# Optimization experiments

Measured on AMD Instinct MI355X. Metric: run time of the kernel, lower is better.

Reference implementation:

```python
import jax, jax.numpy as jnp
import numpy as np

N_NODES = 50000
N_EDGES = 800000
D = 128
N_LAYERS = 3
EPS = 1e-5  # torch LayerNorm default


def _gcn_conv(x, src, dst, dinv, W, b):
    # PyG GCNConv: h = x @ W; out[i] = sum_{(s->i)} dinv[s]*dinv[i]*h[s] + dinv[i]^2*h[i] + b
    h = x @ W
    norm = dinv[src] * dinv[dst]                      # [E]
    msgs = h[src] * norm[:, None]                     # [E, D] gather
    agg = jax.ops.segment_sum(msgs, dst, num_segments=N_NODES)  # scatter-add
    agg = agg + h * (dinv * dinv)[:, None]            # self-loop term
    return agg + b


def _layer_norm(x, gamma, beta):
    mu = jnp.mean(x, axis=-1, keepdims=True)
    var = jnp.mean(jnp.square(x - mu), axis=-1, keepdims=True)
    return (x - mu) * jax.lax.rsqrt(var + EPS) * gamma + beta


def setup_inputs() -> dict:
    key = jax.random.key(0)
    ks = jax.random.split(key, 4)
    x = jax.random.normal(ks[0], (N_NODES, D), dtype=jnp.float32)
    edge_index = jax.random.randint(ks[1], (2, N_EDGES), 0, N_NODES, dtype=jnp.int64)
    Ws = jax.random.normal(ks[2], (N_LAYERS, D, D), dtype=jnp.float32) * (1.0 / np.sqrt(D))
    bs = jnp.zeros((N_LAYERS, D), dtype=jnp.float32)
    gammas = jnp.ones((N_LAYERS, D), dtype=jnp.float32)
    betas = jnp.zeros((N_LAYERS, D), dtype=jnp.float32)
    return {"x": x, "edge_index": edge_index, "Ws": Ws, "bs": bs,
            "gammas": gammas, "betas": betas}


def reference(x, edge_index, Ws, bs, gammas, betas):
    src, dst = edge_index[0], edge_index[1]
    # GCN symmetric normalization with self-loops: deg[i] = in-degree(i) + 1
    deg = jnp.zeros((N_NODES,), dtype=x.dtype).at[dst].add(1.0) + 1.0
    dinv = jax.lax.rsqrt(deg)
    h = x
    for i in range(N_LAYERS):
        x_new = _gcn_conv(h, src, dst, dinv, Ws[i], bs[i])
        x_new = _layer_norm(x_new, gammas[i], betas[i])
        x_new = jax.nn.relu(x_new)  # dropout is identity in eval mode
        h = h + x_new if i > 0 else x_new
    return h
```

## Files before the change

### kernel.cpp

```cpp
#include <hip/hip_runtime.h>
#include <hip/hip_bf16.h>

#define NN 50000
#define NE 800000
#define DD 128
#define NB 196
#define CHSZ 6250
#define NSB 49
#define PH (64 * NB)
#define FS 2048
#define NSL 391
#define HHB (NSL * 8)
#define QB 3125
#define WB 192
#define LG 3125
#define LN_EPS 1e-5f

typedef __bf16 bf16x8 __attribute__((ext_vector_type(8)));
typedef float f32x4 __attribute__((ext_vector_type(4)));

__device__ inline ushort f2bf_bits(float f) {
    union { __hip_bfloat16 h; ushort u; } c;
    c.h = __float2bfloat16(f);
    return c.u;
}

__device__ inline void accum_q16(float* acc, uint4 v, float ww) {
    uint q0 = v.x, q1 = v.y, q2 = v.z, q3 = v.w;
    acc[0]  = fmaf(ww, (float)(char)(q0), acc[0]);
    acc[1]  = fmaf(ww, (float)(char)(q0 >> 8), acc[1]);
    acc[2]  = fmaf(ww, (float)(char)(q0 >> 16), acc[2]);
    acc[3]  = fmaf(ww, (float)(char)(q0 >> 24), acc[3]);
    acc[4]  = fmaf(ww, (float)(char)(q1), acc[4]);
    acc[5]  = fmaf(ww, (float)(char)(q1 >> 8), acc[5]);
    acc[6]  = fmaf(ww, (float)(char)(q1 >> 16), acc[6]);
    acc[7]  = fmaf(ww, (float)(char)(q1 >> 24), acc[7]);
    acc[8]  = fmaf(ww, (float)(char)(q2), acc[8]);
    acc[9]  = fmaf(ww, (float)(char)(q2 >> 8), acc[9]);
    acc[10] = fmaf(ww, (float)(char)(q2 >> 16), acc[10]);
    acc[11] = fmaf(ww, (float)(char)(q2 >> 24), acc[11]);
    acc[12] = fmaf(ww, (float)(char)(q3), acc[12]);
    acc[13] = fmaf(ww, (float)(char)(q3 >> 8), acc[13]);
    acc[14] = fmaf(ww, (float)(char)(q3 >> 16), acc[14]);
    acc[15] = fmaf(ww, (float)(char)(q3 >> 24), acc[15]);
}

__global__ void hist_cast_kernel(const int* __restrict__ dst, int* __restrict__ counts,
                                 int* __restrict__ rank, const float* __restrict__ x,
                                 uint2* __restrict__ qf0, float* __restrict__ sc0,
                                 const float* __restrict__ W, ushort* __restrict__ Wt) {
    int b = blockIdx.x;
    if (b < HHB) {
        int slice = b >> 3;
        int r = b & 7;
        int base = slice * FS;
#pragma unroll 2
        for (int i = threadIdx.x; i < FS; i += 256) {
            int e = base + i;
            if (e < NE) {
                int d = dst[e];
                if (d / CHSZ == r) rank[e] = atomicAdd(&counts[d], 1);
            }
        }
    } else if (b < HHB + QB) {
        int bb = b - HHB;
        int group = threadIdx.x >> 4, t = threadIdx.x & 15;
        int node = bb * 16 + group;
        const float4* xr = (const float4*)(x + (size_t)node * DD + t * 8);
        float4 v0 = xr[0], v1 = xr[1];
        float vals[8] = {v0.x, v0.y, v0.z, v0.w, v1.x, v1.y, v1.z, v1.w};
        float am = 0.f;
#pragma unroll
        for (int i = 0; i < 8; ++i) am = fmaxf(am, fabsf(vals[i]));
#pragma unroll
        for (int off = 1; off <= 8; off <<= 1) am = fmaxf(am, __shfl_xor(am, off, 64));
        float inv = 127.f / fmaxf(am, 1e-20f);
        uint lo = 0, hi = 0;
#pragma unroll
        for (int i = 0; i < 4; ++i) {
            int q = __float2int_rn(vals[i] * inv);
            lo |= ((uint)(q & 0xff)) << (8 * i);
        }
#pragma unroll
        for (int i = 0; i < 4; ++i) {
            int q = __float2int_rn(vals[4 + i] * inv);
            hi |= ((uint)(q & 0xff)) << (8 * i);
        }
        uint2 pk; pk.x = lo; pk.y = hi;
        qf0[node * 16 + t] = pk;
        if (t == 0) sc0[node] = am / 127.f;
    } else {
        int i = (b - HHB - QB) * 256 + threadIdx.x;
        int l = i >> 14, k = (i >> 7) & 127, n = i & 127;
        Wt[l * 16384 + n * 128 + k] = f2bf_bits(W[i]);
    }
}

__global__ __launch_bounds__(1024) void scan1024_blocks(int* __restrict__ data,
                                                        int* __restrict__ bsums) {
    __shared__ int ws[16];
    int gid = blockIdx.x * 1024 + threadIdx.x;
    int lane = threadIdx.x & 63, wid = threadIdx.x >> 6;
    int v = (gid < NN) ? data[gid] : 0;
    int x = v;
#pragma unroll
    for (int off = 1; off < 64; off <<= 1) {
        int t = __shfl_up(x, off, 64);
        if (lane >= off) x += t;
    }
    if (lane == 63) ws[wid] = x;
    __syncthreads();
    if (threadIdx.x == 0) {
        int run = 0;
        for (int i = 0; i < 16; ++i) { int t = ws[i]; ws[i] = run; run += t; }
        bsums[blockIdx.x] = run;
    }
    __syncthreads();
    if (gid < NN) data[gid] = x - v + ws[wid];
}

__global__ __launch_bounds__(1024) void scan_sums1024(int* __restrict__ bsums, int nb) {
    __shared__ int ws[16];
    int tid = threadIdx.x;
    int lane = tid & 63, wid = tid >> 6;
    int v = (tid < nb) ? bsums[tid] : 0;
    int x = v;
#pragma unroll
    for (int off = 1; off < 64; off <<= 1) {
        int t = __shfl_up(x, off, 64);
        if (lane >= off) x += t;
    }
    if (lane == 63) ws[wid] = x;
    __syncthreads();
    if (tid == 0) {
        int run = 0;
        for (int i = 0; i < 16; ++i) { int t = ws[i]; ws[i] = run; run += t; }
    }
    __syncthreads();
    if (tid < nb) bsums[tid] = x - v + ws[wid];
}

__global__ void finalize_kernel(const int* __restrict__ excl, const int* __restrict__ bsums,
                                int* __restrict__ row_ptr, float* __restrict__ dinv,
                                int* __restrict__ degarr, int* __restrict__ bh) {
    __shared__ int lh[64];
    if (threadIdx.x < 64) lh[threadIdx.x] = 0;
    __syncthreads();
    int d = blockIdx.x * 256 + threadIdx.x;
    if (d < NN) {
        int p0 = excl[d] + bsums[d >> 10];
        int nxt = (d == NN - 1) ? NE : excl[d + 1] + bsums[(d + 1) >> 10];
        int deg = nxt - p0;
        row_ptr[d] = p0;
        dinv[d] = rsqrtf((float)deg + 1.0f);
        degarr[d] = deg;
        atomicAdd(&lh[63 - min(deg, 63)], 1);
    }
    __syncthreads();
    if (threadIdx.x < 64) bh[threadIdx.x * NB + blockIdx.x] = lh[threadIdx.x];
    if (blockIdx.x == 0 && threadIdx.x == 0) row_ptr[NN] = NE;
}

__global__ __launch_bounds__(1024) void permscan_kernel(int* __restrict__ bh) {
    __shared__ int wsum[16];
    const int CH = 13;
    int tid = threadIdx.x;
    int base = tid * CH;
    int vals[CH];
    int s = 0;
#pragma unroll
    for (int i = 0; i < CH; ++i) {
        int idx = base + i;
        int v = (idx < PH) ? bh[idx] : 0;
        vals[i] = s;
        s += v;
    }
    int lane = tid & 63, wid = tid >> 6;
    int x = s;
#pragma unroll
    for (int off = 1; off < 64; off <<= 1) {
        int t = __shfl_up(x, off, 64);
        if (lane >= off) x += t;
    }
    if (lane == 63) wsum[wid] = x;
    __syncthreads();
    if (tid == 0) {
        int run = 0;
        for (int i = 0; i < 16; ++i) { int t = wsum[i]; wsum[i] = run; run += t; }
    }
    __syncthreads();
    int texcl = x - s + wsum[wid];
#pragma unroll
    for (int i = 0; i < CH; ++i) {
        int idx = base + i;
        if (idx < PH) bh[idx] = texcl + vals[i];
    }
}

__global__ void scatter_fill_kernel(const int* __restrict__ degarr, const int* __restrict__ bh,
                                    int* __restrict__ perm, const int* __restrict__ src,
                                    const int* __restrict__ dst, const int* __restrict__ excl,
                                    const int* __restrict__ bsums, const int* __restrict__ rank,
                                    const float* __restrict__ dinv, int2* __restrict__ edge2) {
    if (blockIdx.x < NB) {
        __shared__ int lh[64];
        __shared__ int lbase[64];
        if (threadIdx.x < 64) {
            lh[threadIdx.x] = 0;
            lbase[threadIdx.x] = bh[threadIdx.x * NB + blockIdx.x];
        }
        __syncthreads();
        int gid = blockIdx.x * 256 + threadIdx.x;
        if (gid < NN) {
            int b = 63 - min(degarr[gid], 63);
            int r = atomicAdd(&lh[b], 1);
            perm[lbase[b] + r] = gid;
        }
    } else {
        int bb = blockIdx.x - NB;
        if (bb == 0 && threadIdx.x < 8) {
            int2 z; z.x = 0; z.y = 0;
            edge2[NE + threadIdx.x] = z;
        }
        int slice = bb >> 3;
        int r = bb & 7;
        int base = slice * FS;
#pragma unroll 2
        for (int i = threadIdx.x; i < FS; i += 256) {
            int e = base + i;
            if (e < NE) {
                int d = dst[e];
                if (d / CHSZ == r) {
                    int s = src[e];
                    int pos = excl[d] + bsums[d >> 10] + rank[e];
                    int2 o;
                    o.x = s;
                    o.y = __float_as_int(dinv[s] * dinv[d]);
                    edge2[pos] = o;
                }
            }
        }
    }
}

template <bool RES, bool FINAL>
__global__ __launch_bounds__(128) void layer_kernel(
    const uint4* __restrict__ qin, const float* __restrict__ scin,
    const ushort* __restrict__ fin, const int* __restrict__ row_ptr,
    const int2* __restrict__ edge2, const int* __restrict__ perm,
    const float* __restrict__ dinv, const ushort* __restrict__ Wt,
    const float* __restrict__ bias, const float* __restrict__ gamma,
    const float* __restrict__ beta, ushort* __restrict__ fout, char* __restrict__ qfout,
    float* __restrict__ scout, float* __restrict__ out) {
    __shared__ uint4 sA[16 * 17];
    __shared__ int sNode[16];
    __shared__ float sLN1[2][16], sLN2[2][16];
    __shared__ float sMX[2][16];

    int tid = threadIdx.x;
    int wv = tid >> 6, lane = tid & 63;
    int grp = lane >> 3, ln = lane & 7;
    int arow = wv * 8 + grp;
    int slot = blockIdx.x * 16 + arow;
    int node = perm[slot];
    if (ln == 0) sNode[arow] = node;

    {
        int beg = row_ptr[node], deg = row_ptr[node + 1] - beg;
        int nbt = (deg + 7) >> 3;
        float acc[16] = {};

        uint4 qself = qin[node * 8 + ln];
        float wself = dinv[node];
        wself = wself * wself * scin[node];

        const int2* eb = edge2 + beg;
        int bsel = lane & 56;
        for (int b = 0; b < nbt; ++b) {
            int lim = deg - b * 8;
            int2 a = eb[b * 8 + ln];
            float wf = __int_as_float(a.y) * scin[a.x];
            int sj[8];
            float W8[8];
#pragma unroll
            for (int j = 0; j < 8; ++j) sj[j] = __shfl(a.x, bsel + j, 64);
#pragma unroll
            for (int j = 0; j < 8; ++j) W8[j] = __shfl(wf, bsel + j, 64);
            uint4 Q[8];
#pragma unroll
            for (int j = 0; j < 8; ++j) Q[j] = qin[sj[j] * 8 + ln];
#pragma unroll
            for (int j = 0; j < 8; ++j) accum_q16(acc, Q[j], (j < lim) ? W8[j] : 0.f);
        }
        accum_q16(acc, qself, wself);

        union { ushort us[16]; uint4 u[2]; } pk;
#pragma unroll
        for (int i = 0; i < 16; ++i) pk.us[i] = f2bf_bits(acc[i]);
        sA[arow * 17 + 2 * ln] = pk.u[0];
        sA[arow * 17 + 2 * ln + 1] = pk.u[1];
    }
    __syncthreads();

    int q4 = lane >> 4, m = lane & 15;
    f32x4 c0 = (f32x4){0.f, 0.f, 0.f, 0.f};
    f32x4 c1 = c0, c2 = c0, c3 = c0;
    int ncb = 64 * wv;
#pragma unroll
    for (int kk = 0; kk < 4; ++kk) {
        bf16x8 af = *(const bf16x8*)&sA[m * 17 + kk * 4 + q4];
        const ushort* wb = Wt + (size_t)(ncb + m) * DD + kk * 32 + q4 * 8;
        c0 = __builtin_amdgcn_mfma_f32_16x16x32_bf16(af, *(const bf16x8*)(wb), c0, 0, 0, 0);
        c1 = __builtin_amdgcn_mfma_f32_16x16x32_bf16(af, *(const bf16x8*)(wb + 16 * DD), c1, 0, 0, 0);
        c2 = __builtin_amdgcn_mfma_f32_16x16x32_bf16(af, *(const bf16x8*)(wb + 32 * DD), c2, 0, 0, 0);
        c3 = __builtin_amdgcn_mfma_f32_16x16x32_bf16(af, *(const bf16x8*)(wb + 48 * DD), c3, 0, 0, 0);
    }

    float bb0 = bias[ncb + m], bb1 = bias[ncb + 16 + m];
    float bb2 = bias[ncb + 32 + m], bb3 = bias[ncb + 48 + m];
    float s1[4], s2[4];
#pragma unroll
    for (int r = 0; r < 4; ++r) {
        float v0 = c0[r] + bb0, v1 = c1[r] + bb1, v2 = c2[r] + bb2, v3 = c3[r] + bb3;
        c0[r] = v0; c1[r] = v1; c2[r] = v2; c3[r] = v3;
        s1[r] = (v0 + v1) + (v2 + v3);
        s2[r] = (v0 * v0 + v1 * v1) + (v2 * v2 + v3 * v3);
    }
#pragma unroll
    for (int off = 1; off <= 8; off <<= 1) {
#pragma unroll
        for (int r = 0; r < 4; ++r) {
            s1[r] += __shfl_xor(s1[r], off, 64);
            s2[r] += __shfl_xor(s2[r], off, 64);
        }
    }
    if (m == 0) {
#pragma unroll
        for (int r = 0; r < 4; ++r) {
            sLN1[wv][q4 * 4 + r] = s1[r];
            sLN2[wv][q4 * 4 + r] = s2[r];
        }
    }
    __syncthreads();
    float ga0 = gamma[ncb + m], ga1 = gamma[ncb + 16 + m];
    float ga2 = gamma[ncb + 32 + m], ga3 = gamma[ncb + 48 + m];
    float be0 = beta[ncb + m], be1 = beta[ncb + 16 + m];
    float be2 = beta[ncb + 32 + m], be3 = beta[ncb + 48 + m];
    float o0v[4], o1v[4], o2v[4], o3v[4], rmax[4];
#pragma unroll
    for (int r = 0; r < 4; ++r) {
        int row = q4 * 4 + r;
        float S1 = sLN1[0][row] + sLN1[1][row];
        float S2 = sLN2[0][row] + sLN2[1][row];
        float mu = S1 * (1.f / 128.f);
        float var = S2 * (1.f / 128.f) - mu * mu;
        float rstd = rsqrtf(var + LN_EPS);
        int nd = sNode[row];
        size_t rb = (size_t)nd * DD;
        float o0 = fmaxf((c0[r] - mu) * rstd * ga0 + be0, 0.f);
        float o1 = fmaxf((c1[r] - mu) * rstd * ga1 + be1, 0.f);
        float o2 = fmaxf((c2[r] - mu) * rstd * ga2 + be2, 0.f);
        float o3 = fmaxf((c3[r] - mu) * rstd * ga3 + be3, 0.f);
        if (RES) {
            o0 += __uint_as_float(((uint)fin[rb + ncb + m]) << 16);
            o1 += __uint_as_float(((uint)fin[rb + ncb + 16 + m]) << 16);
            o2 += __uint_as_float(((uint)fin[rb + ncb + 32 + m]) << 16);
            o3 += __uint_as_float(((uint)fin[rb + ncb + 48 + m]) << 16);
        }
        if (FINAL) {
            out[rb + ncb + m] = o0;
            out[rb + ncb + 16 + m] = o1;
            out[rb + ncb + 32 + m] = o2;
            out[rb + ncb + 48 + m] = o3;
        } else {
            fout[rb + ncb + m] = f2bf_bits(o0);
            fout[rb + ncb + 16 + m] = f2bf_bits(o1);
            fout[rb + ncb + 32 + m] = f2bf_bits(o2);
            fout[rb + ncb + 48 + m] = f2bf_bits(o3);
            o0v[r] = o0; o1v[r] = o1; o2v[r] = o2; o3v[r] = o3;
            rmax[r] = fmaxf(fmaxf(o0, o1), fmaxf(o2, o3));
        }
    }
    if (!FINAL) {
#pragma unroll
        for (int off = 1; off <= 8; off <<= 1) {
#pragma unroll
            for (int r = 0; r < 4; ++r) rmax[r] = fmaxf(rmax[r], __shfl_xor(rmax[r], off, 64));
        }
        if (m == 0) {
#pragma unroll
            for (int r = 0; r < 4; ++r) sMX[wv][q4 * 4 + r] = rmax[r];
        }
        __syncthreads();
#pragma unroll
        for (int r = 0; r < 4; ++r) {
            int row = q4 * 4 + r;
            float M = fmaxf(sMX[0][row], sMX[1][row]);
            float inv = 127.f / fmaxf(M, 1e-20f);
            int nd = sNode[row];
            if (wv == 0 && m == 0) scout[nd] = M / 127.f;
            size_t rb = (size_t)nd * DD;
            int q0 = min(__float2int_rn(o0v[r] * inv), 127);
            int q1 = min(__float2int_rn(o1v[r] * inv), 127);
            int q2 = min(__float2int_rn(o2v[r] * inv), 127);
            int q3 = min(__float2int_rn(o3v[r] * inv), 127);
            qfout[rb + ncb + m] = (char)q0;
            qfout[rb + ncb + 16 + m] = (char)q1;
            qfout[rb + ncb + 32 + m] = (char)q2;
            qfout[rb + ncb + 48 + m] = (char)q3;
        }
    }
}


extern "C" void kernel_launch(void* const* d_in, const int* in_sizes, int n_in,
                              void* d_out, int out_size, void* d_ws, size_t ws_size,
                              hipStream_t stream) {
    const float* x = (const float*)d_in[0];
    const int* edge = (const int*)d_in[1];
    const float* Ws = (const float*)d_in[2];
    const float* bs = (const float*)d_in[3];
    const float* gs = (const float*)d_in[4];
    const float* bes = (const float*)d_in[5];
    float* out = (float*)d_out;
    const int* src = edge;
    const int* dst = edge + NE;

    char* p = (char*)d_ws;
    int* counts = (int*)p;      p += (size_t)NN * 4;
    int* bsums = (int*)p;       p += 1024 * 4;
    int* row_ptr = (int*)p;     p += (size_t)(NN + 4) * 4;
    int* rank = (int*)p;        p += (size_t)NE * 4;
    float* dinv = (float*)p;    p += (size_t)NN * 4;
    int* degarr = (int*)p;      p += (size_t)NN * 4;
    int* bh = (int*)p;          p += (size_t)PH * 4;
    int* perm = (int*)p;        p += (size_t)NN * 4;
    int2* edge2 = (int2*)p;     p += (size_t)(NE + 8) * 8;
    ushort* fb0 = (ushort*)p;   p += (size_t)NN * DD * 2;
    ushort* fb1 = (ushort*)p;   p += (size_t)NN * DD * 2;
    char* qf0 = (char*)p;       p += (size_t)NN * DD;
    char* qf1 = (char*)p;       p += (size_t)NN * DD;
    float* sc0 = (float*)p;     p += (size_t)NN * 4;
    float* sc1 = (float*)p;     p += (size_t)NN * 4;
    ushort* Wt = (ushort*)p;    p += (size_t)3 * DD * DD * 2;

    hipMemsetAsync(counts, 0, (size_t)NN * 4, stream);
    hist_cast_kernel<<<HHB + QB + WB, 256, 0, stream>>>(dst, counts, rank, x,
                                                        (uint2*)qf0, sc0, Ws, Wt);
    scan1024_blocks<<<NSB, 1024, 0, stream>>>(counts, bsums);
    scan_sums1024<<<1, 1024, 0, stream>>>(bsums, NSB);
    finalize_kernel<<<NB, 256, 0, stream>>>(counts, bsums, row_ptr, dinv, degarr, bh);
    permscan_kernel<<<1, 1024, 0, stream>>>(bh);
    scatter_fill_kernel<<<NB + NSL * 8, 256, 0, stream>>>(degarr, bh, perm, src, dst, counts,
                                                          bsums, rank, dinv, edge2);

    layer_kernel<false, false><<<LG, 128, 0, stream>>>(
        (const uint4*)qf0, sc0, fb0, row_ptr, edge2, perm, dinv, Wt, bs, gs, bes,
        fb1, qf1, sc1, out);
    layer_kernel<true, false><<<LG, 128, 0, stream>>>(
        (const uint4*)qf1, sc1, fb1, row_ptr, edge2, perm, dinv, Wt + 16384, bs + DD, gs + DD,
        bes + DD, fb0, qf0, sc0, out);
    layer_kernel<true, true><<<LG, 128, 0, stream>>>(
        (const uint4*)qf0, sc0, fb0, row_ptr, edge2, perm, dinv, Wt + 32768, bs + 2 * DD,
        gs + 2 * DD, bes + 2 * DD, fb1, qf1, sc1, out);
}
```

Measured before the change: 289.8 us.

## Switch int8 feature quantization from per-node to global per-tensor scale

Replaces the per-node int8 scale with a single per-tensor max-abs scale, computed by atomicMax reductions. The gather loop no longer loads a per-neighbor scale, and the scale is applied once to the accumulator before the bf16 conversion. Quantization now runs in separate quant kernels that read the bf16 features after each layer, which adds extra launches and an extra pass over memory. A global scale coarsens precision for rows with small magnitudes, so accuracy becomes a risk.

```diff
diff --git a/kernel.cpp b/kernel.cpp
--- a/kernel.cpp
+++ b/kernel.cpp
@@ -11,7 +11,7 @@
 #define FS 2048
 #define NSL 391
 #define HHB (NSL * 8)
-#define QB 3125
+#define AB 256
 #define WB 192
 #define LG 3125
 #define LN_EPS 1e-5f
@@ -47,8 +47,9 @@
 
 __global__ void hist_cast_kernel(const int* __restrict__ dst, int* __restrict__ counts,
                                  int* __restrict__ rank, const float* __restrict__ x,
-                                 uint2* __restrict__ qf0, float* __restrict__ sc0,
-                                 const float* __restrict__ W, ushort* __restrict__ Wt) {
+                                 int* __restrict__ amax0, const float* __restrict__ W,
+                                 ushort* __restrict__ Wt) {
+    __shared__ float sam[4];
     int b = blockIdx.x;
     if (b < HHB) {
         int slice = b >> 3;
@@ -62,38 +63,78 @@
                 if (d / CHSZ == r) rank[e] = atomicAdd(&counts[d], 1);
             }
         }
-    } else if (b < HHB + QB) {
+    } else if (b < HHB + AB) {
         int bb = b - HHB;
-        int group = threadIdx.x >> 4, t = threadIdx.x & 15;
-        int node = bb * 16 + group;
-        const float4* xr = (const float4*)(x + (size_t)node * DD + t * 8);
-        float4 v0 = xr[0], v1 = xr[1];
-        float vals[8] = {v0.x, v0.y, v0.z, v0.w, v1.x, v1.y, v1.z, v1.w};
+        const float4* xv = (const float4*)x;
         float am = 0.f;
-#pragma unroll
-        for (int i = 0; i < 8; ++i) am = fmaxf(am, fabsf(vals[i]));
-#pragma unroll
-        for (int off = 1; off <= 8; off <<= 1) am = fmaxf(am, __shfl_xor(am, off, 64));
-        float inv = 127.f / fmaxf(am, 1e-20f);
-        uint lo = 0, hi = 0;
-#pragma unroll
-        for (int i = 0; i < 4; ++i) {
-            int q = __float2int_rn(vals[i] * inv);
-            lo |= ((uint)(q & 0xff)) << (8 * i);
-        }
-#pragma unroll
-        for (int i = 0; i < 4; ++i) {
-            int q = __float2int_rn(vals[4 + i] * inv);
-            hi |= ((uint)(q & 0xff)) << (8 * i);
-        }
-        uint2 pk; pk.x = lo; pk.y = hi;
-        qf0[node * 16 + t] = pk;
-        if (t == 0) sc0[node] = am / 127.f;
+        for (int i = bb * 256 + threadIdx.x; i < NN * DD / 4; i += AB * 256) {
+            float4 v = xv[i];
+            am = fmaxf(fmaxf(fabsf(v.x), fabsf(v.y)),
+                       fmaxf(fmaxf(fabsf(v.z), fabsf(v.w)), am));
+        }
+#pragma unroll
+        for (int off = 1; off <= 32; off <<= 1) am = fmaxf(am, __shfl_xor(am, off, 64));
+        int lane = threadIdx.x & 63, wv = threadIdx.x >> 6;
+        if (lane == 0) sam[wv] = am;
+        __syncthreads();
+        if (threadIdx.x == 0) {
+            float m = fmaxf(fmaxf(sam[0], sam[1]), fmaxf(sam[2], sam[3]));
+            atomicMax(amax0, __float_as_int(m));
+        }
     } else {
-        int i = (b - HHB - QB) * 256 + threadIdx.x;
+        int i = (b - HHB - AB) * 256 + threadIdx.x;
         int l = i >> 14, k = (i >> 7) & 127, n = i & 127;
         Wt[l * 16384 + n * 128 + k] = f2bf_bits(W[i]);
     }
+}
+
+__global__ __launch_bounds__(256) void quant_x_kernel(const float* __restrict__ x,
+                                                      const int* __restrict__ amax,
+                                                      uint2* __restrict__ qf) {
+    int i = blockIdx.x * 256 + threadIdx.x;
+    float inv = 127.f / fmaxf(__int_as_float(*amax), 1e-20f);
+    const float4* xr = (const float4*)x + (size_t)i * 2;
+    float4 v0 = xr[0], v1 = xr[1];
+    float vals[8] = {v0.x, v0.y, v0.z, v0.w, v1.x, v1.y, v1.z, v1.w};
+    uint lo = 0, hi = 0;
+#pragma unroll
+    for (int j = 0; j < 4; ++j) {
+        int q = min(__float2int_rn(vals[j] * inv), 127);
+        lo |= ((uint)(q & 0xff)) << (8 * j);
+    }
+#pragma unroll
+    for (int j = 0; j < 4; ++j) {
+        int q = min(__float2int_rn(vals[4 + j] * inv), 127);
+        hi |= ((uint)(q & 0xff)) << (8 * j);
+    }
+    uint2 pk; pk.x = lo; pk.y = hi;
+    qf[i] = pk;
+}
+
+__global__ __launch_bounds__(256) void quant_h_kernel(const uint4* __restrict__ fin,
+                                                      const int* __restrict__ amax,
+                                                      uint2* __restrict__ qf) {
+    int i = blockIdx.x * 256 + threadIdx.x;
+    float inv = 127.f / fmaxf(__int_as_float(*amax), 1e-20f);
+    uint4 v = fin[i];
+    float vals[8] = {
+        __uint_as_float(v.x << 16), __uint_as_float(v.x & 0xffff0000u),
+        __uint_as_float(v.y << 16), __uint_as_float(v.y & 0xffff0000u),
+        __uint_as_float(v.z << 16), __uint_as_float(v.z & 0xffff0000u),
+        __uint_as_float(v.w << 16), __uint_as_float(v.w & 0xffff0000u)};
+    uint lo = 0, hi = 0;
+#pragma unroll
+    for (int j = 0; j < 4; ++j) {
+        int q = min(__float2int_rn(vals[j] * inv), 127);
+        lo |= ((uint)(q & 0xff)) << (8 * j);
+    }
+#pragma unroll
+    for (int j = 0; j < 4; ++j) {
+        int q = min(__float2int_rn(vals[4 + j] * inv), 127);
+        hi |= ((uint)(q & 0xff)) << (8 * j);
+    }
+    uint2 pk; pk.x = lo; pk.y = hi;
+    qf[i] = pk;
 }
 
 __global__ __launch_bounds__(1024) void scan1024_blocks(int* __restrict__ data,
@@ -245,17 +286,17 @@
 
 template <bool RES, bool FINAL>
 __global__ __launch_bounds__(128) void layer_kernel(
-    const uint4* __restrict__ qin, const float* __restrict__ scin,
+    const uint4* __restrict__ qin, const int* __restrict__ amax_in,
     const ushort* __restrict__ fin, const int* __restrict__ row_ptr,
     const int2* __restrict__ edge2, const int* __restrict__ perm,
     const float* __restrict__ dinv, const ushort* __restrict__ Wt,
     const float* __restrict__ bias, const float* __restrict__ gamma,
-    const float* __restrict__ beta, ushort* __restrict__ fout, char* __restrict__ qfout,
-    float* __restrict__ scout, float* __restrict__ out) {
+    const float* __restrict__ beta, ushort* __restrict__ fout,
+    int* __restrict__ amax_out, float* __restrict__ out) {
     __shared__ uint4 sA[16 * 17];
     __shared__ int sNode[16];
     __shared__ float sLN1[2][16], sLN2[2][16];
-    __shared__ float sMX[2][16];
+    __shared__ float sMXr[2];
 
     int tid = threadIdx.x;
     int wv = tid >> 6, lane = tid & 63;
@@ -265,6 +306,8 @@
     int node = perm[slot];
     if (ln == 0) sNode[arow] = node;
 
+    float scg = __int_as_float(*amax_in) * (1.f / 127.f);
+
     {
         int beg = row_ptr[node], deg = row_ptr[node + 1] - beg;
         int nbt = (deg + 7) >> 3;
@@ -272,20 +315,19 @@
 
         uint4 qself = qin[node * 8 + ln];
         float wself = dinv[node];
-        wself = wself * wself * scin[node];
+        wself = wself * wself;
 
         const int2* eb = edge2 + beg;
         int bsel = lane & 56;
         for (int b = 0; b < nbt; ++b) {
             int lim = deg - b * 8;
             int2 a = eb[b * 8 + ln];
-            float wf = __int_as_float(a.y) * scin[a.x];
             int sj[8];
             float W8[8];
 #pragma unroll
             for (int j = 0; j < 8; ++j) sj[j] = __shfl(a.x, bsel + j, 64);
 #pragma unroll
-            for (int j = 0; j < 8; ++j) W8[j] = __shfl(wf, bsel + j, 64);
+            for (int j = 0; j < 8; ++j) W8[j] = __int_as_float(__shfl(a.y, bsel + j, 64));
             uint4 Q[8];
 #pragma unroll
             for (int j = 0; j < 8; ++j) Q[j] = qin[sj[j] * 8 + ln];
@@ -296,7 +338,7 @@
 
         union { ushort us[16]; uint4 u[2]; } pk;
 #pragma unroll
-        for (int i = 0; i < 16; ++i) pk.us[i] = f2bf_bits(acc[i]);
+        for (int i = 0; i < 16; ++i) pk.us[i] = f2bf_bits(acc[i] * scg);
         sA[arow * 17 + 2 * ln] = pk.u[0];
         sA[arow * 17 + 2 * ln + 1] = pk.u[1];
     }
@@ -346,7 +388,7 @@
     float ga2 = gamma[ncb + 32 + m], ga3 = gamma[ncb + 48 + m];
     float be0 = beta[ncb + m], be1 = beta[ncb + 16 + m];
     float be2 = beta[ncb + 32 + m], be3 = beta[ncb + 48 + m];
-    float o0v[4], o1v[4], o2v[4], o3v[4], rmax[4];
+    float vmax = 0.f;
 #pragma unroll
     for (int r = 0; r < 4; ++r) {
         int row = q4 * 4 + r;
@@ -377,38 +419,15 @@
             fout[rb + ncb + 16 + m] = f2bf_bits(o1);
             fout[rb + ncb + 32 + m] = f2bf_bits(o2);
             fout[rb + ncb + 48 + m] = f2bf_bits(o3);
-            o0v[r] = o0; o1v[r] = o1; o2v[r] = o2; o3v[r] = o3;
-            rmax[r] = fmaxf(fmaxf(o0, o1), fmaxf(o2, o3));
+            vmax = fmaxf(vmax, fmaxf(fmaxf(o0, o1), fmaxf(o2, o3)));
         }
     }
     if (!FINAL) {
 #pragma unroll
-        for (int off = 1; off <= 8; off <<= 1) {
-#pragma unroll
-            for (int r = 0; r < 4; ++r) rmax[r] = fmaxf(rmax[r], __shfl_xor(rmax[r], off, 64));
-        }
-        if (m == 0) {
-#pragma unroll
-            for (int r = 0; r < 4; ++r) sMX[wv][q4 * 4 + r] = rmax[r];
-        }
+        for (int off = 1; off <= 32; off <<= 1) vmax = fmaxf(vmax, __shfl_xor(vmax, off, 64));
+        if (lane == 0) sMXr[wv] = vmax;
         __syncthreads();
-#pragma unroll
-        for (int r = 0; r < 4; ++r) {
-            int row = q4 * 4 + r;
-            float M = fmaxf(sMX[0][row], sMX[1][row]);
-            float inv = 127.f / fmaxf(M, 1e-20f);
-            int nd = sNode[row];
-            if (wv == 0 && m == 0) scout[nd] = M / 127.f;
-            size_t rb = (size_t)nd * DD;
-            int q0 = min(__float2int_rn(o0v[r] * inv), 127);
-            int q1 = min(__float2int_rn(o1v[r] * inv), 127);
-            int q2 = min(__float2int_rn(o2v[r] * inv), 127);
-            int q3 = min(__float2int_rn(o3v[r] * inv), 127);
-            qfout[rb + ncb + m] = (char)q0;
-            qfout[rb + ncb + 16 + m] = (char)q1;
-            qfout[rb + ncb + 32 + m] = (char)q2;
-            qfout[rb + ncb + 48 + m] = (char)q3;
-        }
+        if (tid == 0) atomicMax(amax_out, __float_as_int(fmaxf(sMXr[0], sMXr[1])));
     }
 }
 
@@ -428,6 +447,7 @@
 
     char* p = (char*)d_ws;
     int* counts = (int*)p;      p += (size_t)NN * 4;
+    int* amax = (int*)p;        p += 4 * 4;
     int* bsums = (int*)p;       p += 1024 * 4;
     int* row_ptr = (int*)p;     p += (size_t)(NN + 4) * 4;
     int* rank = (int*)p;        p += (size_t)NE * 4;
@@ -440,27 +460,27 @@
     ushort* fb1 = (ushort*)p;   p += (size_t)NN * DD * 2;
     char* qf0 = (char*)p;       p += (size_t)NN * DD;
     char* qf1 = (char*)p;       p += (size_t)NN * DD;
-    float* sc0 = (float*)p;     p += (size_t)NN * 4;
-    float* sc1 = (float*)p;     p += (size_t)NN * 4;
     ushort* Wt = (ushort*)p;    p += (size_t)3 * DD * DD * 2;
 
-    hipMemsetAsync(counts, 0, (size_t)NN * 4, stream);
-    hist_cast_kernel<<<HHB + QB + WB, 256, 0, stream>>>(dst, counts, rank, x,
-                                                        (uint2*)qf0, sc0, Ws, Wt);
+    hipMemsetAsync(counts, 0, (size_t)NN * 4 + 16, stream);
+    hist_cast_kernel<<<HHB + AB + WB, 256, 0, stream>>>(dst, counts, rank, x, amax, Ws, Wt);
     scan1024_blocks<<<NSB, 1024, 0, stream>>>(counts, bsums);
     scan_sums1024<<<1, 1024, 0, stream>>>(bsums, NSB);
     finalize_kernel<<<NB, 256, 0, stream>>>(counts, bsums, row_ptr, dinv, degarr, bh);
     permscan_kernel<<<1, 1024, 0, stream>>>(bh);
     scatter_fill_kernel<<<NB + NSL * 8, 256, 0, stream>>>(degarr, bh, perm, src, dst, counts,
                                                           bsums, rank, dinv, edge2);
+    quant_x_kernel<<<LG, 256, 0, stream>>>(x, amax, (uint2*)qf0);
 
     layer_kernel<false, false><<<LG, 128, 0, stream>>>(
-        (const uint4*)qf0, sc0, fb0, row_ptr, edge2, perm, dinv, Wt, bs, gs, bes,
-        fb1, qf1, sc1, out);
+        (const uint4*)qf0, amax, fb0, row_ptr, edge2, perm, dinv, Wt, bs, gs, bes,
+        fb1, amax + 1, out);
+    quant_h_kernel<<<LG, 256, 0, stream>>>((const uint4*)fb1, amax + 1, (uint2*)qf1);
     layer_kernel<true, false><<<LG, 128, 0, stream>>>(
-        (const uint4*)qf1, sc1, fb1, row_ptr, edge2, perm, dinv, Wt + 16384, bs + DD, gs + DD,
-        bes + DD, fb0, qf0, sc0, out);
+        (const uint4*)qf1, amax + 1, fb1, row_ptr, edge2, perm, dinv, Wt + 16384, bs + DD,
+        gs + DD, bes + DD, fb0, amax + 2, out);
+    quant_h_kernel<<<LG, 256, 0, stream>>>((const uint4*)fb0, amax + 2, (uint2*)qf0);
     layer_kernel<true, true><<<LG, 128, 0, stream>>>(
-        (const uint4*)qf0, sc0, fb0, row_ptr, edge2, perm, dinv, Wt + 32768, bs + 2 * DD,
-        gs + 2 * DD, bes + 2 * DD, fb1, qf1, sc1, out);
-}
+        (const uint4*)qf0, amax + 2, fb0, row_ptr, edge2, perm, dinv, Wt + 32768, bs + 2 * DD,
+        gs + 2 * DD, bes + 2 * DD, fb1, amax + 3, out);
+}
```

New measurement: 331.5 us. +14.4%, slower.
